# Kernel optimization log

Measured on AMD Instinct MI355X. Metric: run time of the kernel, lower is better.

The kernel has to match this reference:

```python
import jax, jax.numpy as jnp
import numpy as np
from jax import lax

CHUNK = 512  # query-point chunk for pairwise point-triangle distance
EPS = 1e-12
LOSS_WEIGHT = 1.0


def closest_point_on_tri(p, a, b, c):
    """Closest point on triangle (a,b,c) to p. Broadcasts over leading dims; last dim = 3.
    Ericson, Real-Time Collision Detection, ch. 5.1.5."""
    ab = b - a
    ac = c - a
    ap = p - a
    d1 = (ab * ap).sum(-1)
    d2 = (ac * ap).sum(-1)
    bp = p - b
    d3 = (ab * bp).sum(-1)
    d4 = (ac * bp).sum(-1)
    cp_ = p - c
    d5 = (ab * cp_).sum(-1)
    d6 = (ac * cp_).sum(-1)
    va = d3 * d6 - d5 * d4
    vb = d5 * d2 - d1 * d6
    vc = d1 * d4 - d3 * d2
    # edge / interior parameters (denominators guarded; masks pick valid regions)
    v_ab = (d1 / jnp.maximum(d1 - d3, EPS))[..., None]
    w_ac = (d2 / jnp.maximum(d2 - d6, EPS))[..., None]
    w_bc = ((d4 - d3) / jnp.maximum((d4 - d3) + (d5 - d6), EPS))[..., None]
    denom = jnp.maximum(va + vb + vc, EPS)
    v_in = (vb / denom)[..., None]
    w_in = (vc / denom)[..., None]
    cond1 = ((d1 <= 0) & (d2 <= 0))[..., None]            # vertex a
    cond2 = ((d3 >= 0) & (d4 <= d3))[..., None]           # vertex b
    cond3 = ((d6 >= 0) & (d5 <= d6))[..., None]           # vertex c
    cond4 = ((vc <= 0) & (d1 >= 0) & (d3 <= 0))[..., None]  # edge ab
    cond5 = ((vb <= 0) & (d2 >= 0) & (d6 <= 0))[..., None]  # edge ac
    cond6 = ((va <= 0) & ((d4 - d3) >= 0) & ((d5 - d6) >= 0))[..., None]  # edge bc
    out = a + ab * v_in + ac * w_in                      # interior
    out = jnp.where(cond6, b + (c - b) * w_bc, out)
    out = jnp.where(cond5, a + ac * w_ac, out)
    out = jnp.where(cond4, a + ab * v_ab, out)
    out = jnp.where(cond3, c, out)
    out = jnp.where(cond2, b, out)
    out = jnp.where(cond1, a, out)
    return out


def nearest_points_on_mesh(points, verts, faces):
    """Exact nearest point on mesh surface for each query point.
    points: [P,3], verts: [V,3], faces: [F,3] int. Returns cp [P,3]."""
    ta = verts[faces[:, 0]]  # [F,3]
    tb = verts[faces[:, 1]]
    tc = verts[faces[:, 2]]

    def chunk_argmin(pc):  # pc: [CHUNK,3]
        cp = closest_point_on_tri(pc[:, None, :], ta[None], tb[None], tc[None])  # [C,F,3]
        d2 = ((pc[:, None, :] - cp) ** 2).sum(-1)  # [C,F]
        return jnp.argmin(d2, axis=1)

    P = points.shape[0]
    idx = lax.map(chunk_argmin, points.reshape(-1, CHUNK, 3)).reshape(P)
    cp = closest_point_on_tri(points, ta[idx], tb[idx], tc[idx])  # [P,3]
    return cp


def _per_batch_loss(points, verts, faces):
    cp = nearest_points_on_mesh(points, verts, faces)
    # torch.norm(resid, p=2) is the Frobenius norm of the whole [P,3] residual (scalar);
    # closest point is detached in the original autograd.Function usage.
    resid = points - lax.stop_gradient(cp)
    dist = jnp.sqrt((resid ** 2).sum())
    height = verts[:, 1].max() - verts[:, 1].min()  # bbox_3d[1]
    return dist / height


def setup_inputs() -> dict:
    key = jax.random.key(0)
    k1, k2, k3 = jax.random.split(key, 3)
    B, P, V, F = 2, 8192, 4098, 8192
    body_verts = jax.random.normal(k1, (B, P, 3), dtype=jnp.float32)
    mesh_verts = jax.random.normal(k2, (B, V, 3), dtype=jnp.float32)
    faces = jax.random.randint(k3, (B, F, 3), 0, V, dtype=jnp.int32)
    return {"body_verts": body_verts, "mesh_verts": mesh_verts, "faces": faces}


def reference(body_verts, mesh_verts, faces):
    losses = jax.vmap(_per_batch_loss)(body_verts, mesh_verts, faces)  # [B]
    return jnp.mean(losses) * LOSS_WEIGHT
```

## Files before the change

### kernel.cpp

```cpp
#include <hip/hip_runtime.h>

#define EPSF 1e-12f
constexpr int BB = 2;
constexpr int PP = 8192;
constexpr int VV = 4098;
constexpr int FF = 8192;

constexpr int FAST_F4 = 7;
constexpr int SLOW_F4 = 5;
constexpr int PTS_PER_BLOCK = 2048;
constexpr int NSLICES = 128;
constexpr int CHUNK_T = FF / NSLICES;

typedef float f2 __attribute__((ext_vector_type(2)));

__device__ __forceinline__ f2 vfma(f2 a, f2 b, f2 c) {
#if __has_builtin(__builtin_elementwise_fma)
    return __builtin_elementwise_fma(a, b, c);
#else
    return (f2){fmaf(a.x, b.x, c.x), fmaf(a.y, b.y, c.y)};
#endif
}
__device__ __forceinline__ f2 vmin2(f2 a, f2 b) { return __builtin_elementwise_min(a, b); }
__device__ __forceinline__ f2 vmax2(f2 a, f2 b) { return __builtin_elementwise_max(a, b); }
__device__ __forceinline__ f2 bc(float s) { return (f2){s, s}; }

__global__ __launch_bounds__(256) void precompute_kernel(
    const float* __restrict__ verts, const int* __restrict__ faces,
    float4* __restrict__ fastrec, float4* __restrict__ slowrec,
    unsigned long long* __restrict__ mask, unsigned int* __restrict__ minD,
    float* __restrict__ out)
{
    int idx = blockIdx.x * 256 + threadIdx.x;
    if (idx == 0) out[0] = 0.0f;
    if (idx < BB * PP) minD[idx] = 0x7F800000u;
    if (idx >= BB * FF) return;

    int b = idx / FF;
    const float* vb = verts + (size_t)b * VV * 3;
    int i0 = faces[idx * 3 + 0];
    int i1 = faces[idx * 3 + 1];
    int i2 = faces[idx * 3 + 2];

    float ax = vb[i0*3+0], ay = vb[i0*3+1], az = vb[i0*3+2];
    float bx = vb[i1*3+0], by = vb[i1*3+1], bz = vb[i1*3+2];
    float cx = vb[i2*3+0], cy = vb[i2*3+1], cz = vb[i2*3+2];

    float abx = bx-ax, aby = by-ay, abz = bz-az;
    float acx = cx-ax, acy = cy-ay, acz = cz-az;
    float bcx = cx-bx, bcy = cy-by, bcz = cz-bz;

    {
        float4* t = slowrec + (size_t)idx * SLOW_F4;
        t[0] = make_float4(ax, ay, az, abx);
        t[1] = make_float4(bx, by, bz, aby);
        t[2] = make_float4(cx, cy, cz, abz);
        t[3] = make_float4(acx, acy, acz, bcx);
        t[4] = make_float4(bcy, bcz, 0.0f, 0.0f);
    }

    float nx = aby*acz - abz*acy;
    float ny = abz*acx - abx*acz;
    float nz = abx*acy - aby*acx;

    float ka1 = abx*ax + aby*ay + abz*az;
    float ka2 = acx*ax + acy*ay + acz*az;
    float kb1 = abx*bx + aby*by + abz*bz;
    float kb2 = acx*bx + acy*by + acz*bz;
    float kc1 = abx*cx + aby*cy + abz*cz;
    float kc2 = acx*cx + acy*cy + acz*cz;
    float kan = nx*ax + ny*ay + nz*az;
    float aa  = ax*ax + ay*ay + az*az;

    float ab2 = abx*abx + aby*aby + abz*abz;
    float ac2 = acx*acx + acy*acy + acz*acz;
    float bc2 = bcx*bcx + bcy*bcy + bcz*bcz;
    float nn  = nx*nx + ny*ny + nz*nz;

    float inv_ab2 = 1.0f / fmaxf(ab2, EPSF);
    float inv_ac2 = 1.0f / fmaxf(ac2, EPSF);
    float inv_bc2 = 1.0f / fmaxf(bc2, EPSF);
    float inv_nn  = 1.0f / fmaxf(nn,  EPSF);

    bool slowtri = !((nn > 0.03f * (ab2 * ac2)) &&
                     (ab2 > 1e-4f) && (ac2 > 1e-4f) && (bc2 > 1e-4f));

    unsigned long long mb = __ballot(slowtri);
    if ((threadIdx.x & 63) == 0) mask[idx >> 6] = mb;

    float INF = __uint_as_float(0x7F800000u);
    float4* f = fastrec + (size_t)idx * FAST_F4;
    f[0] = make_float4(abx, aby, abz, ka1);
    f[1] = make_float4(acx, acy, acz, ka2);
    f[2] = make_float4(nx,  ny,  nz,  slowtri ? INF : kan);
    f[3] = make_float4(ax,  ay,  az,  slowtri ? INF : aa);
    f[4] = make_float4(kb1, kb2, kc1, kc2);
    f[5] = make_float4(inv_ab2, inv_ac2, inv_bc2, inv_nn);
    f[6] = make_float4(ab2, ac2, bc2, 0.0f);
}

__device__ __forceinline__ float tri_d2(
    float px, float py, float pz,
    float4 R0, float4 R1, float4 R2, float4 R3, float4 R4)
{
#pragma clang fp contract(off)
    float ax = R0.x, ay = R0.y, az = R0.z;
    float bx = R1.x, by = R1.y, bz = R1.z;
    float cx = R2.x, cy = R2.y, cz = R2.z;
    float abx = R0.w, aby = R1.w, abz = R2.w;
    float acx = R3.x, acy = R3.y, acz = R3.z;
    float bcx = R3.w, bcy = R4.x, bcz = R4.y;

    float apx = px - ax, apy = py - ay, apz = pz - az;
    float d1 = (abx*apx + aby*apy) + abz*apz;
    float d2 = (acx*apx + acy*apy) + acz*apz;
    float bpx = px - bx, bpy = py - by, bpz = pz - bz;
    float d3 = (abx*bpx + aby*bpy) + abz*bpz;
    float d4 = (acx*bpx + acy*bpy) + acz*bpz;
    float cqx = px - cx, cqy = py - cy, cqz = pz - cz;
    float d5 = (abx*cqx + aby*cqy) + abz*cqz;
    float d6 = (acx*cqx + acy*cqy) + acz*cqz;

    float va = d3*d6 - d5*d4;
    float vb = d5*d2 - d1*d6;
    float vc = d1*d4 - d3*d2;
    float u43 = d4 - d3;
    float u56 = d5 - d6;

    bool c1 = (d1 <= 0.0f) && (d2 <= 0.0f);
    bool c2 = (d3 >= 0.0f) && (d4 <= d3);
    bool c3 = (d6 >= 0.0f) && (d5 <= d6);
    bool c4 = (vc <= 0.0f) && (d1 >= 0.0f) && (d3 <= 0.0f);
    bool c5 = (vb <= 0.0f) && (d2 >= 0.0f) && (d6 <= 0.0f);
    bool c6 = (va <= 0.0f) && (u43 >= 0.0f) && (u56 >= 0.0f);

    int reg = c1 ? 0 : (c2 ? 1 : (c3 ? 2 : (c4 ? 3 : (c5 ? 4 : (c6 ? 5 : 6)))));

    float denom = fmaxf((va + vb) + vc, EPSF);
    float den1 = (reg == 3) ? fmaxf(d1 - d3, EPSF)
               : (reg == 5) ? fmaxf(u43 + u56, EPSF)
               : (reg == 6) ? denom : 1.0f;
    float num1 = (reg == 3) ? d1
               : (reg == 5) ? u43
               : (reg == 6) ? vb : 0.0f;
    float den2 = (reg == 4) ? fmaxf(d2 - d6, EPSF)
               : (reg == 6) ? denom : 1.0f;
    float num2 = (reg == 4) ? d2
               : (reg == 6) ? vc : 0.0f;
    float s = num1 / den1;
    float t = num2 / den2;

    bool useB = (reg == 1) || (reg == 5);
    bool useC = (reg == 2);
    float basex = useB ? bx : (useC ? cx : ax);
    float basey = useB ? by : (useC ? cy : ay);
    float basez = useB ? bz : (useC ? cz : az);
    bool e1bc = (reg == 5);
    float e1x = e1bc ? bcx : abx;
    float e1y = e1bc ? bcy : aby;
    float e1z = e1bc ? bcz : abz;

    float cpx = (basex + e1x*s) + acx*t;
    float cpy = (basey + e1y*s) + acy*t;
    float cpz = (basez + e1z*s) + acz*t;
    float rx = px - cpx, ry = py - cpy, rz = pz - cpz;
    return (rx*rx + ry*ry) + rz*rz;
}

__device__ __forceinline__ f2 fast_d2_pk(
    f2 px, f2 py, f2 pz, f2 pp,
    float4 F0, float4 F1, float4 F2, float4 F3, float4 F4, float4 F5, float4 F6)
{
    const float INF = __uint_as_float(0x7F800000u);

    f2 sab = vfma(bc(F0.x), px, vfma(bc(F0.y), py, bc(F0.z) * pz));
    f2 sac = vfma(bc(F1.x), px, vfma(bc(F1.y), py, bc(F1.z) * pz));
    f2 sn  = vfma(bc(F2.x), px, vfma(bc(F2.y), py, bc(F2.z) * pz));
    f2 adp = vfma(bc(F3.x), px, vfma(bc(F3.y), py, bc(F3.z) * pz));

    f2 d1 = sab - bc(F0.w), d2 = sac - bc(F1.w);
    f2 d3 = sab - bc(F4.x), d4 = sac - bc(F4.y);
    f2 d5 = sab - bc(F4.z), d6 = sac - bc(F4.w);
    f2 tp = sn - bc(F2.w);

    f2 ap2 = vfma(bc(-2.0f), adp, pp) + bc(F3.w);
    f2 bp2 = vfma(bc(-2.0f), d1, ap2) + bc(F6.x);

    f2 sA = vmin2(vmax2(d1 * bc(F5.x), bc(0.0f)), bc(1.0f));
    f2 dAB = vfma(-sA, vfma(-sA, bc(F6.x), d1 + d1), ap2);
    f2 sC = vmin2(vmax2(d2 * bc(F5.y), bc(0.0f)), bc(1.0f));
    f2 dAC = vfma(-sC, vfma(-sC, bc(F6.y), d2 + d2), ap2);
    f2 u43 = d4 - d3;
    f2 sB = vmin2(vmax2(u43 * bc(F5.z), bc(0.0f)), bc(1.0f));
    f2 dBC = vfma(-sB, vfma(-sB, bc(F6.z), u43 + u43), bp2);

    f2 va = vfma(d3, d6, -(d5 * d4));
    f2 vb = vfma(d5, d2, -(d1 * d6));
    f2 vc = vfma(d1, d4, -(d3 * d2));
    f2 dIN = (tp * tp) * bc(F5.w);

    f2 dI;
    dI.x = (va.x >= 0.0f && vb.x >= 0.0f && vc.x >= 0.0f) ? dIN.x : INF;
    dI.y = (va.y >= 0.0f && vb.y >= 0.0f && vc.y >= 0.0f) ? dIN.y : INF;

    return vmin2(vmin2(dAB, dAC), vmin2(dBC, dI));
}

__global__ __launch_bounds__(256) void dist_kernel(
    const float* __restrict__ pts, const float4* __restrict__ fa,
    const float4* __restrict__ sa, const unsigned long long* __restrict__ mask,
    unsigned int* __restrict__ minD)
{
    int tid   = threadIdx.x;
    int pg    = blockIdx.x;
    int slice = blockIdx.y;

    int b  = pg / (PP / PTS_PER_BLOCK);
    int p0 = pg * PTS_PER_BLOCK + tid;

    f2 px[4], py[4], pz[4], pp[4], m[4];
    int pidx[8];
#pragma unroll
    for (int k = 0; k < 4; ++k) {
        int pa = p0 + (2*k)   * 256;
        int pb = p0 + (2*k+1) * 256;
        pidx[2*k] = pa; pidx[2*k+1] = pb;
        px[k] = (f2){pts[pa*3+0], pts[pb*3+0]};
        py[k] = (f2){pts[pa*3+1], pts[pb*3+1]};
        pz[k] = (f2){pts[pa*3+2], pts[pb*3+2]};
        pp[k] = vfma(px[k], px[k], vfma(py[k], py[k], pz[k] * pz[k]));
        m[k] = bc(__uint_as_float(0x7F800000u));
    }

    int t0 = b * FF + slice * CHUNK_T;
    const float4* fb = fa + (size_t)t0 * FAST_F4;

    for (int t = 0; t < CHUNK_T; ++t) {
        float4 F0 = fb[t*FAST_F4+0];
        float4 F1 = fb[t*FAST_F4+1];
        float4 F2 = fb[t*FAST_F4+2];
        float4 F3 = fb[t*FAST_F4+3];
        float4 F4 = fb[t*FAST_F4+4];
        float4 F5 = fb[t*FAST_F4+5];
        float4 F6 = fb[t*FAST_F4+6];
#pragma unroll
        for (int k = 0; k < 4; ++k)
            m[k] = vmin2(m[k], fast_d2_pk(px[k], py[k], pz[k], pp[k],
                                          F0, F1, F2, F3, F4, F5, F6));
    }

    unsigned long long bits = mask[t0 >> 6];
    while (bits) {
        int bit = __builtin_ctzll(bits);
        bits &= bits - 1;
        const float4* sb = sa + (size_t)(t0 + bit) * SLOW_F4;
        float4 S0 = sb[0], S1 = sb[1], S2 = sb[2], S3 = sb[3], S4 = sb[4];
#pragma unroll
        for (int k = 0; k < 4; ++k) {
            m[k].x = fminf(m[k].x, tri_d2(px[k].x, py[k].x, pz[k].x, S0, S1, S2, S3, S4));
            m[k].y = fminf(m[k].y, tri_d2(px[k].y, py[k].y, pz[k].y, S0, S1, S2, S3, S4));
        }
    }

#pragma unroll
    for (int k = 0; k < 4; ++k) {
        atomicMin(&minD[pidx[2*k]],   __float_as_uint(fmaxf(m[k].x, 0.0f)));
        atomicMin(&minD[pidx[2*k+1]], __float_as_uint(fmaxf(m[k].y, 0.0f)));
    }
}

__global__ __launch_bounds__(256) void reduce_kernel(
    const unsigned int* __restrict__ minD, const float* __restrict__ verts,
    float* __restrict__ out)
{
    int b = blockIdx.x;
    int tid = threadIdx.x;

    float s = 0.0f;
    for (int i = tid; i < PP; i += 256)
        s += __uint_as_float(minD[b * PP + i]);

    float ymin = 3.4e38f, ymax = -3.4e38f;
    for (int i = tid; i < VV; i += 256) {
        float y = verts[((size_t)b * VV + i) * 3 + 1];
        ymin = fminf(ymin, y); ymax = fmaxf(ymax, y);
    }

    for (int off = 32; off > 0; off >>= 1) {
        s += __shfl_down(s, off);
        ymin = fminf(ymin, __shfl_down(ymin, off));
        ymax = fmaxf(ymax, __shfl_down(ymax, off));
    }

    __shared__ float shs[4], shmn[4], shmx[4];
    if ((tid & 63) == 0) {
        int w = tid >> 6;
        shs[w] = s; shmn[w] = ymin; shmx[w] = ymax;
    }
    __syncthreads();
    if (tid == 0) {
        float tot = shs[0], mn = shmn[0], mx = shmx[0];
        for (int w = 1; w < 4; ++w) {
            tot += shs[w];
            mn = fminf(mn, shmn[w]);
            mx = fmaxf(mx, shmx[w]);
        }
        atomicAdd(out, 0.5f * sqrtf(tot) / (mx - mn));
    }
}

extern "C" void kernel_launch(void* const* d_in, const int* in_sizes, int n_in,
                              void* d_out, int out_size, void* d_ws, size_t ws_size,
                              hipStream_t stream) {
    const float* pts   = (const float*)d_in[0];
    const float* verts = (const float*)d_in[1];
    const int*   faces = (const int*)d_in[2];
    float* out = (float*)d_out;

    char* w = (char*)d_ws;
    float4* fastrec = (float4*)w;
    w += (size_t)BB * FF * FAST_F4 * sizeof(float4);
    float4* slowrec = (float4*)w;
    w += (size_t)BB * FF * SLOW_F4 * sizeof(float4);
    unsigned long long* mask = (unsigned long long*)w;
    w += (size_t)(BB * FF / 64) * sizeof(unsigned long long);
    unsigned int* minD = (unsigned int*)w;

    precompute_kernel<<<(BB * FF + 255) / 256, 256, 0, stream>>>(
        verts, faces, fastrec, slowrec, mask, minD, out);

    dim3 grid(BB * PP / PTS_PER_BLOCK, NSLICES);
    dist_kernel<<<grid, 256, 0, stream>>>(pts, fastrec, slowrec, mask, minD);

    reduce_kernel<<<BB, 256, 0, stream>>>(minD, verts, out);
}
```

Measured before the change: 236.6 us.

## Shrink fast triangle record to six float4s and double face slices

Each triangle's fast record now holds edge-length and edge-dot terms instead of the per-vertex projection constants. d3..d6 are derived from d1/d2 using ab2, ac2 and ab·ac, which cuts one float4 load per triangle and reduces record size. The interior test is collapsed into a min of va/vb/vc, and the face slice count is doubled to raise grid parallelism. Because CHUNK_T is now 32, the slow-triangle mask is shifted and masked to the slice's 32 bits. The cost is more atomicMin traffic and a slightly different rounding path for the derived d3..d6.

```diff
diff --git a/kernel.cpp b/kernel.cpp
--- a/kernel.cpp
+++ b/kernel.cpp
@@ -6,10 +6,10 @@
 constexpr int VV = 4098;
 constexpr int FF = 8192;
 
-constexpr int FAST_F4 = 7;
+constexpr int FAST_F4 = 6;
 constexpr int SLOW_F4 = 5;
 constexpr int PTS_PER_BLOCK = 2048;
-constexpr int NSLICES = 128;
+constexpr int NSLICES = 256;
 constexpr int CHUNK_T = FF / NSLICES;
 
 typedef float f2 __attribute__((ext_vector_type(2)));
@@ -63,14 +63,11 @@
     float ny = abz*acx - abx*acz;
     float nz = abx*acy - aby*acx;
 
-    float ka1 = abx*ax + aby*ay + abz*az;
-    float ka2 = acx*ax + acy*ay + acz*az;
-    float kb1 = abx*bx + aby*by + abz*bz;
-    float kb2 = acx*bx + acy*by + acz*bz;
-    float kc1 = abx*cx + aby*cy + abz*cz;
-    float kc2 = acx*cx + acy*cy + acz*cz;
-    float kan = nx*ax + ny*ay + nz*az;
-    float aa  = ax*ax + ay*ay + az*az;
+    float ka1  = abx*ax + aby*ay + abz*az;
+    float ka2  = acx*ax + acy*ay + acz*az;
+    float kan  = nx*ax + ny*ay + nz*az;
+    float aa   = ax*ax + ay*ay + az*az;
+    float abac = abx*acx + aby*acy + abz*acz;
 
     float ab2 = abx*abx + aby*aby + abz*abz;
     float ac2 = acx*acx + acy*acy + acz*acz;
@@ -94,9 +91,8 @@
     f[1] = make_float4(acx, acy, acz, ka2);
     f[2] = make_float4(nx,  ny,  nz,  slowtri ? INF : kan);
     f[3] = make_float4(ax,  ay,  az,  slowtri ? INF : aa);
-    f[4] = make_float4(kb1, kb2, kc1, kc2);
+    f[4] = make_float4(ab2, ac2, abac, bc2);
     f[5] = make_float4(inv_ab2, inv_ac2, inv_bc2, inv_nn);
-    f[6] = make_float4(ab2, ac2, bc2, 0.0f);
 }
 
 __device__ __forceinline__ float tri_d2(
@@ -169,7 +165,7 @@
 
 __device__ __forceinline__ f2 fast_d2_pk(
     f2 px, f2 py, f2 pz, f2 pp,
-    float4 F0, float4 F1, float4 F2, float4 F3, float4 F4, float4 F5, float4 F6)
+    float4 F0, float4 F1, float4 F2, float4 F3, float4 F4, float4 F5)
 {
     const float INF = __uint_as_float(0x7F800000u);
 
@@ -179,29 +175,32 @@
     f2 adp = vfma(bc(F3.x), px, vfma(bc(F3.y), py, bc(F3.z) * pz));
 
     f2 d1 = sab - bc(F0.w), d2 = sac - bc(F1.w);
-    f2 d3 = sab - bc(F4.x), d4 = sac - bc(F4.y);
-    f2 d5 = sab - bc(F4.z), d6 = sac - bc(F4.w);
+    f2 d3 = d1 - bc(F4.x);
+    f2 d4 = d2 - bc(F4.z);
+    f2 d5 = d1 - bc(F4.z);
+    f2 d6 = d2 - bc(F4.y);
     f2 tp = sn - bc(F2.w);
 
     f2 ap2 = vfma(bc(-2.0f), adp, pp) + bc(F3.w);
-    f2 bp2 = vfma(bc(-2.0f), d1, ap2) + bc(F6.x);
+    f2 bp2 = vfma(bc(-2.0f), d1, ap2) + bc(F4.x);
 
     f2 sA = vmin2(vmax2(d1 * bc(F5.x), bc(0.0f)), bc(1.0f));
-    f2 dAB = vfma(-sA, vfma(-sA, bc(F6.x), d1 + d1), ap2);
+    f2 dAB = vfma(-sA, vfma(-sA, bc(F4.x), d1 + d1), ap2);
     f2 sC = vmin2(vmax2(d2 * bc(F5.y), bc(0.0f)), bc(1.0f));
-    f2 dAC = vfma(-sC, vfma(-sC, bc(F6.y), d2 + d2), ap2);
+    f2 dAC = vfma(-sC, vfma(-sC, bc(F4.y), d2 + d2), ap2);
     f2 u43 = d4 - d3;
     f2 sB = vmin2(vmax2(u43 * bc(F5.z), bc(0.0f)), bc(1.0f));
-    f2 dBC = vfma(-sB, vfma(-sB, bc(F6.z), u43 + u43), bp2);
+    f2 dBC = vfma(-sB, vfma(-sB, bc(F4.w), u43 + u43), bp2);
 
     f2 va = vfma(d3, d6, -(d5 * d4));
     f2 vb = vfma(d5, d2, -(d1 * d6));
     f2 vc = vfma(d1, d4, -(d3 * d2));
+    f2 mv = vmin2(vmin2(va, vb), vc);
     f2 dIN = (tp * tp) * bc(F5.w);
 
     f2 dI;
-    dI.x = (va.x >= 0.0f && vb.x >= 0.0f && vc.x >= 0.0f) ? dIN.x : INF;
-    dI.y = (va.y >= 0.0f && vb.y >= 0.0f && vc.y >= 0.0f) ? dIN.y : INF;
+    dI.x = (mv.x >= 0.0f) ? dIN.x : INF;
+    dI.y = (mv.y >= 0.0f) ? dIN.y : INF;
 
     return vmin2(vmin2(dAB, dAC), vmin2(dBC, dI));
 }
@@ -242,14 +241,14 @@
         float4 F3 = fb[t*FAST_F4+3];
         float4 F4 = fb[t*FAST_F4+4];
         float4 F5 = fb[t*FAST_F4+5];
-        float4 F6 = fb[t*FAST_F4+6];
 #pragma unroll
         for (int k = 0; k < 4; ++k)
             m[k] = vmin2(m[k], fast_d2_pk(px[k], py[k], pz[k], pp[k],
-                                          F0, F1, F2, F3, F4, F5, F6));
-    }
-
-    unsigned long long bits = mask[t0 >> 6];
+                                          F0, F1, F2, F3, F4, F5));
+    }
+
+    unsigned long long bits =
+        (mask[t0 >> 6] >> (t0 & 63)) & 0xFFFFFFFFull;
     while (bits) {
         int bit = __builtin_ctzll(bits);
         bits &= bits - 1;
```

Result: faster. 217.0 us (-8.3%).
